# Kernel optimization log

Measured on AMD Instinct MI355X. Metric: run time of the kernel, lower is better.

## Reference

```python
import jax, jax.numpy as jnp
import numpy as np

HEADS = 8
D_MODEL = 512
NU = 1
EPS = 1e-6
SEQ = 4096
BATCH = 8
DK = D_MODEL // HEADS          # 64
PHI = 2 * NU * DK              # 128, DPFP output dim


def dpfp(x):
    """Deterministic Parameter-Free Projection, then L1 normalize."""
    x = jnp.concatenate([jax.nn.relu(x), jax.nn.relu(-x)], axis=-1)  # [..., 2*dk]
    x_rolled = jnp.concatenate([jnp.roll(x, j, axis=-1) for j in range(1, NU + 1)], axis=-1)
    x_repeat = jnp.concatenate([x] * NU, axis=-1)
    y = x_repeat * x_rolled                                          # [..., 2*nu*dk]
    return y / (jnp.sum(y, axis=-1, keepdims=True) + EPS)


def setup_inputs() -> dict:
    key = jax.random.key(0)
    ks = jax.random.split(key, 7)
    s = 0.02
    return {
        "x": jax.random.normal(ks[0], (SEQ, BATCH, D_MODEL), dtype=jnp.float32),
        "Wq": jax.random.normal(ks[1], (D_MODEL, HEADS * DK), dtype=jnp.float32) * s,
        "Wk": jax.random.normal(ks[2], (D_MODEL, HEADS * DK), dtype=jnp.float32) * s,
        "Wv": jax.random.normal(ks[3], (D_MODEL, HEADS * DK), dtype=jnp.float32) * s,
        "Wg": jax.random.normal(ks[4], (D_MODEL, HEADS), dtype=jnp.float32) * s,
        "Wo": jax.random.normal(ks[5], (D_MODEL, D_MODEL), dtype=jnp.float32) * s,
        "bo": jnp.zeros((D_MODEL,), dtype=jnp.float32),
    }


def reference(x, Wq, Wk, Wv, Wg, Wo, bo):
    S, B, D = x.shape
    q = dpfp((x @ Wq).reshape(S, B, HEADS, DK))            # [S,B,H,PHI]
    k = dpfp((x @ Wk).reshape(S, B, HEADS, DK))            # [S,B,H,PHI]
    v = (x @ Wv).reshape(S, B, HEADS, DK)                  # [S,B,H,DK]
    beta = jax.nn.sigmoid((x @ Wg).reshape(S, B, HEADS, 1))  # [S,B,H,1]

    def step(W, qkvb):
        qi, ki, vi, bi = qkvb                              # [B,H,PHI],[B,H,PHI],[B,H,DK],[B,H,1]
        v_exist = jnp.einsum('bhvk,bhk->bhv', W, ki)       # delta-rule read
        W = W + jnp.einsum('bhv,bhk->bhvk', bi * (vi - v_exist), ki)
        out = jnp.einsum('bhvk,bhk->bhv', W, qi)
        return W, out

    W0 = jnp.zeros((B, HEADS, DK, PHI), dtype=x.dtype)
    _, outs = jax.lax.scan(step, W0, (q, k, v, beta))      # outs: [S,B,H,DK]
    out = outs.reshape(S, B, HEADS * DK)
    return out @ Wo + bo
```

## Files before the change

kernel.cpp:

```cpp
#include <hip/hip_runtime.h>

#define SEQ 4096
#define BATCH 8
#define HEADS 8
#define DMODEL 512
#define DK 64
#define PHI 128
#define CHUNK 1024
#define CROWS (CHUNK * BATCH)
#define SB 32
#define NSB (CHUNK / SB)

__device__ __forceinline__ void async16(const float* g, float* l)
{
    __builtin_amdgcn_global_load_lds((const __attribute__((address_space(1))) void*)g,
                                     (__attribute__((address_space(3))) void*)l, 16, 0, 0);
}
__device__ __forceinline__ void async4(const float* g, float* l)
{
    __builtin_amdgcn_global_load_lds((const __attribute__((address_space(1))) void*)g,
                                     (__attribute__((address_space(3))) void*)l, 4, 0, 0);
}

__device__ __forceinline__ float rowsum16(float x)
{
    x += __int_as_float(__builtin_amdgcn_update_dpp(0, __float_as_int(x), 0x121, 0xF, 0xF, true));
    x += __int_as_float(__builtin_amdgcn_update_dpp(0, __float_as_int(x), 0x122, 0xF, 0xF, true));
    x += __int_as_float(__builtin_amdgcn_update_dpp(0, __float_as_int(x), 0x124, 0xF, 0xF, true));
    x += __int_as_float(__builtin_amdgcn_update_dpp(0, __float_as_int(x), 0x128, 0xF, 0xF, true));
    return x;
}

__device__ __forceinline__ float dot8(const float4 x0, const float4 x1,
                                      const float4 y0, const float4 y1)
{
    float a  = x0.x * y0.x;
    float b2 = x1.x * y1.x;
    a = fmaf(x0.y, y0.y, a); b2 = fmaf(x1.y, y1.y, b2);
    a = fmaf(x0.z, y0.z, a); b2 = fmaf(x1.z, y1.z, b2);
    a = fmaf(x0.w, y0.w, a); b2 = fmaf(x1.w, y1.w, b2);
    return a + b2;
}

__global__ __launch_bounds__(256)
void transpose_kernel(const float* __restrict__ X, float* __restrict__ XT)
{
    __shared__ float tile[64][65];
    const int t  = threadIdx.x;
    const int tx = t & 15;
    const int ty = t >> 4;
    const int bm = blockIdx.x * 64;
    const int bn = blockIdx.y * 64;
#pragma unroll
    for (int i = 0; i < 4; ++i) {
        const int r = ty + i * 16;
        const float4 v = *(const float4*)(X + (size_t)(bm + r) * 512 + bn + tx * 4);
        tile[r][tx * 4 + 0] = v.x; tile[r][tx * 4 + 1] = v.y;
        tile[r][tx * 4 + 2] = v.z; tile[r][tx * 4 + 3] = v.w;
    }
    __syncthreads();
#pragma unroll
    for (int i = 0; i < 4; ++i) {
        const int r = ty + i * 16;
        float4 v;
        v.x = tile[tx * 4 + 0][r];
        v.y = tile[tx * 4 + 1][r];
        v.z = tile[tx * 4 + 2][r];
        v.w = tile[tx * 4 + 3][r];
        *(float4*)(XT + (size_t)(bn + r) * CROWS + bm + tx * 4) = v;
    }
}

__global__ __launch_bounds__(256)
void gemm_qkv(const float* __restrict__ AT,
              const float* __restrict__ Wq, const float* __restrict__ Wk,
              const float* __restrict__ Wv,
              float* __restrict__ Qp, float* __restrict__ Kp, float* __restrict__ Vd)
{
    __shared__ __align__(16) float As[2][16][128];
    __shared__ __align__(16) float Bs[2][16][128];
    const int t  = threadIdx.x;
    const int tx = t & 15;
    const int ty = t >> 4;
    const int bm  = blockIdx.x * 128;
    const int grp = blockIdx.y >> 2;
    const int bn  = (blockIdx.y & 3) * 128;
    const float* B = (grp == 0) ? Wq : (grp == 1) ? Wk : Wv;

    float acc[8][8];
#pragma unroll
    for (int i = 0; i < 8; ++i)
#pragma unroll
        for (int j = 0; j < 8; ++j) acc[i][j] = 0.f;

    auto stage = [&](int buf, int kt) {
        const int k0 = kt * 16;
#pragma unroll
        for (int i = 0; i < 2; ++i) {
            const int L = t + i * 256;
            const int k = L >> 5, c4 = L & 31;
            async16(AT + (size_t)(k0 + k) * CROWS + bm + c4 * 4,
                    &As[buf][0][0] + L * 4);
            async16(B + (size_t)(k0 + k) * 512 + bn + c4 * 4,
                    &Bs[buf][0][0] + L * 4);
        }
    };

    stage(0, 0);
    for (int kt = 0; kt < 32; ++kt) {
        const int buf = kt & 1;
        __syncthreads();
        if (kt + 1 < 32) stage(buf ^ 1, kt + 1);
#pragma unroll
        for (int k = 0; k < 16; ++k) {
            float af[8], bf[8];
            *(float4*)&af[0] = *(const float4*)&As[buf][k][ty * 8];
            *(float4*)&af[4] = *(const float4*)&As[buf][k][ty * 8 + 4];
            *(float4*)&bf[0] = *(const float4*)&Bs[buf][k][tx * 4];
            *(float4*)&bf[4] = *(const float4*)&Bs[buf][k][64 + tx * 4];
#pragma unroll
            for (int i = 0; i < 8; ++i)
#pragma unroll
                for (int j = 0; j < 8; ++j)
                    acc[i][j] = fmaf(af[i], bf[j], acc[i][j]);
        }
    }

    if (grp < 2) {
        float* dst = grp ? Kp : Qp;
        const int ln  = t & 63;
        const int lnp = (ln & 48) | ((ln + 15) & 15);
        const int hA  = bn >> 6;
#pragma unroll
        for (int hh = 0; hh < 2; ++hh) {
            const int h = hA + hh;
#pragma unroll
            for (int i = 0; i < 8; ++i) {
                const int m = bm + ty * 8 + i;
                float ap[4], an[4];
#pragma unroll
                for (int j = 0; j < 4; ++j) {
                    const float v = acc[i][hh * 4 + j];
                    ap[j] = fmaxf(v, 0.f);
                    an[j] = fmaxf(-v, 0.f);
                }
                const float sap = __shfl(ap[3], lnp);
                const float san = __shfl(an[3], lnp);
                const float p0  = (tx == 0) ? san : sap;
                const float p64 = (tx == 0) ? sap : san;
                float y0[4], y1[4];
                y0[0] = ap[0] * p0;    y1[0] = an[0] * p64;
                y0[1] = ap[1] * ap[0]; y1[1] = an[1] * an[0];
                y0[2] = ap[2] * ap[1]; y1[2] = an[2] * an[1];
                y0[3] = ap[3] * ap[2]; y1[3] = an[3] * an[2];
                float s = (y0[0] + y0[1] + y0[2] + y0[3]) + (y1[0] + y1[1] + y1[2] + y1[3]);
                s = rowsum16(s);
                const float inv = 1.f / (s + 1e-6f);
                float4 o0, o1;
                o0.x = y0[0] * inv; o0.y = y0[1] * inv; o0.z = y0[2] * inv; o0.w = y0[3] * inv;
                o1.x = y1[0] * inv; o1.y = y1[1] * inv; o1.z = y1[2] * inv; o1.w = y1[3] * inv;
                *(float4*)(dst + (size_t)m * 1024 + h * 128 + tx * 4)      = o0;
                *(float4*)(dst + (size_t)m * 1024 + h * 128 + 64 + tx * 4) = o1;
            }
        }
    } else {
#pragma unroll
        for (int i = 0; i < 8; ++i) {
            const int m = bm + ty * 8 + i;
            float4 o0, o1;
            o0.x = acc[i][0]; o0.y = acc[i][1]; o0.z = acc[i][2]; o0.w = acc[i][3];
            o1.x = acc[i][4]; o1.y = acc[i][5]; o1.z = acc[i][6]; o1.w = acc[i][7];
            *(float4*)(Vd + (size_t)m * 512 + bn + tx * 4)      = o0;
            *(float4*)(Vd + (size_t)m * 512 + bn + 64 + tx * 4) = o1;
        }
    }
}

__global__ __launch_bounds__(256)
void gemm_wo(const float* __restrict__ AT, const float* __restrict__ B,
             const float* __restrict__ bias, float* __restrict__ C)
{
    __shared__ __align__(16) float As[2][32][128];
    __shared__ __align__(16) float Bs[2][32][64];
    const int t  = threadIdx.x;
    const int tx = t & 15;
    const int ty = t >> 4;
    const int bm = blockIdx.x * 128;
    const int bn = blockIdx.y * 64;

    float acc[8][4];
#pragma unroll
    for (int i = 0; i < 8; ++i)
#pragma unroll
        for (int j = 0; j < 4; ++j) acc[i][j] = 0.f;

    auto stage = [&](int buf, int kt) {
        const int k0 = kt * 32;
#pragma unroll
        for (int i = 0; i < 4; ++i) {
            const int L = t + i * 256;
            const int k = L >> 5, c4 = L & 31;
            async16(AT + (size_t)(k0 + k) * CROWS + bm + c4 * 4,
                    &As[buf][0][0] + L * 4);
        }
#pragma unroll
        for (int i = 0; i < 2; ++i) {
            const int L = t + i * 256;
            const int k = L >> 4, c4 = L & 15;
            async16(B + (size_t)(k0 + k) * 512 + bn + c4 * 4,
                    &Bs[buf][0][0] + L * 4);
        }
    };

    stage(0, 0);
    for (int kt = 0; kt < 16; ++kt) {
        const int buf = kt & 1;
        __syncthreads();
        if (kt + 1 < 16) stage(buf ^ 1, kt + 1);
#pragma unroll
        for (int k = 0; k < 32; ++k) {
            float af[8], bf[4];
            *(float4*)&af[0] = *(const float4*)&As[buf][k][ty * 8];
            *(float4*)&af[4] = *(const float4*)&As[buf][k][ty * 8 + 4];
            *(float4*)&bf[0] = *(const float4*)&Bs[buf][k][tx * 4];
#pragma unroll
            for (int i = 0; i < 8; ++i)
#pragma unroll
                for (int j = 0; j < 4; ++j)
                    acc[i][j] = fmaf(af[i], bf[j], acc[i][j]);
        }
    }

#pragma unroll
    for (int i = 0; i < 8; ++i) {
        const int m = bm + ty * 8 + i;
        float4 o;
        o.x = acc[i][0]; o.y = acc[i][1]; o.z = acc[i][2]; o.w = acc[i][3];
        const float4 bb = *(const float4*)(bias + bn + tx * 4);
        o.x += bb.x; o.y += bb.y; o.z += bb.z; o.w += bb.w;
        *(float4*)(C + (size_t)m * 512 + bn + tx * 4) = o;
    }
}

__global__ __launch_bounds__(256)
void gemm_g_kernel(const float* __restrict__ X, const float* __restrict__ Wg,
                   float* __restrict__ Bt)
{
    const int idx = blockIdx.x * 256 + threadIdx.x;
    const int row = idx >> 3;
    const int c   = idx & 7;
    const float4* x4 = (const float4*)(X + (size_t)row * DMODEL);
    float acc = 0.f;
    for (int k4 = 0; k4 < 128; ++k4) {
        const float4 xv = x4[k4];
        acc = fmaf(xv.x, Wg[(k4 * 4 + 0) * 8 + c], acc);
        acc = fmaf(xv.y, Wg[(k4 * 4 + 1) * 8 + c], acc);
        acc = fmaf(xv.z, Wg[(k4 * 4 + 2) * 8 + c], acc);
        acc = fmaf(xv.w, Wg[(k4 * 4 + 3) * 8 + c], acc);
    }
    Bt[idx] = 1.f / (1.f + expf(-acc));
}

__global__ __launch_bounds__(256)
void scan_kernel(const float* __restrict__ Qp, const float* __restrict__ Kp,
                 const float* __restrict__ Vd, const float* __restrict__ Bt,
                 float* __restrict__ outsT, float* __restrict__ Wst,
                 int s0, int first)
{
    const int blk = blockIdx.x;
    const int bh  = blk & 63;
    const int rg  = blk >> 6;
    const int b   = bh >> 3;
    const int h   = bh & 7;
    const int t   = threadIdx.x;
    const int c      = t & 15;
    const int rloc   = t >> 4;
    const int wv  = t >> 6;
    const int ln  = t & 63;

    __shared__ __align__(16) float sk[2][SB][PHI];
    __shared__ __align__(16) float sq[2][SB][PHI];
    __shared__ __align__(16) float sv[2][SB][16];
    __shared__ __align__(16) float sb2[2][SB];
    __shared__ __align__(16) float sd[2][SB][4];

    const size_t bh128 = (size_t)(b * 8 + h) * 128;

    float w[8];
    float* wslot = Wst + (size_t)blk * 2048 + t * 8;
    if (first) {
#pragma unroll
        for (int j = 0; j < 8; ++j) w[j] = 0.f;
    } else {
        const float4 w0 = *(const float4*)(wslot);
        const float4 w1 = *(const float4*)(wslot + 4);
        w[0] = w0.x; w[1] = w0.y; w[2] = w0.z; w[3] = w0.w;
        w[4] = w1.x; w[5] = w1.y; w[6] = w1.z; w[7] = w1.w;
    }

    auto stage = [&](int sbuf, int sb) {
        const int sqb = sb * SB;
        if (wv < 2) {
#pragma unroll
            for (int i = 0; i < 8; ++i) {
                const int L  = i * 128 + wv * 64 + ln;
                const int sl = L >> 5, c4 = L & 31;
                async16(Kp + (size_t)(sqb + sl) * 8192 + bh128 + c4 * 4,
                        &sk[sbuf][0][0] + L * 4);
            }
            {
                const int L  = wv * 64 + ln;
                const int sl = L >> 2, c4 = L & 3;
                async16(Vd + (size_t)(sqb + sl) * 4096 + b * 512 + h * 64 + rg * 16 + c4 * 4,
                        &sv[sbuf][0][0] + L * 4);
            }
        } else {
#pragma unroll
            for (int i = 0; i < 8; ++i) {
                const int L  = i * 128 + (wv - 2) * 64 + ln;
                const int sl = L >> 5, c4 = L & 31;
                async16(Qp + (size_t)(sqb + sl) * 8192 + bh128 + c4 * 4,
                        &sq[sbuf][0][0] + L * 4);
            }
            if (wv == 2 && ln < SB) {
                async4(Bt + (size_t)(s0 + sqb + ln) * 64 + b * 8 + h,
                       &sb2[sbuf][0] + ln);
            }
        }
    };

    auto dots_phase = [&](int buf, int sb) {
        const int sl0 = 2 * rloc;
        const float* kmp = (rloc == 0) ? &sk[buf ^ 1][SB - 1][0] : &sk[buf][sl0 - 1][0];
        const float4 km0 = *(const float4*)(kmp + 4 * c);
        const float4 km1 = *(const float4*)(kmp + 64 + 4 * c);
        const float4 ka0 = *(const float4*)&sk[buf][sl0][4 * c];
        const float4 ka1 = *(const float4*)&sk[buf][sl0][64 + 4 * c];
        const float4 kb0 = *(const float4*)&sk[buf][sl0 + 1][4 * c];
        const float4 kb1 = *(const float4*)&sk[buf][sl0 + 1][64 + 4 * c];
        const float4 qa0 = *(const float4*)&sq[buf][sl0][4 * c];
        const float4 qa1 = *(const float4*)&sq[buf][sl0][64 + 4 * c];
        const float4 qb0 = *(const float4*)&sq[buf][sl0 + 1][4 * c];
        const float4 qb1 = *(const float4*)&sq[buf][sl0 + 1][64 + 4 * c];
        const float kk_a  = rowsum16(dot8(km0, km1, ka0, ka1));
        const float kq1_a = rowsum16(dot8(km0, km1, qa0, qa1));
        const float kq0_a = rowsum16(dot8(ka0, ka1, qa0, qa1));
        const float kk_b  = rowsum16(dot8(ka0, ka1, kb0, kb1));
        const float kq1_b = rowsum16(dot8(ka0, ka1, qb0, qb1));
        const float kq0_b = rowsum16(dot8(kb0, kb1, qb0, qb1));
        if (c == 0) {
            const bool z = (sb == 0) && (rloc == 0);
            sd[buf][sl0][0] = z ? 0.f : kk_a;
            sd[buf][sl0][1] = z ? 0.f : kq1_a;
            sd[buf][sl0][2] = kq0_a;
            sd[buf][sl0][3] = sb2[buf][sl0];
            sd[buf][sl0 + 1][0] = kk_b;
            sd[buf][sl0 + 1][1] = kq1_b;
            sd[buf][sl0 + 1][2] = kq0_b;
            sd[buf][sl0 + 1][3] = sb2[buf][sl0 + 1];
        }
    };

    struct Frag { float4 k0, k1, q0, q1; float bb, bv, kk, kq1, kq0; };
    Frag r[8];
    float d_prev = 0.f;

    auto preload = [&](Frag& f, int sbuf, int sl) {
        f.k0 = *(const float4*)&sk[sbuf][sl][4 * c];
        f.k1 = *(const float4*)&sk[sbuf][sl][64 + 4 * c];
        f.q0 = *(const float4*)&sq[sbuf][sl][4 * c];
        f.q1 = *(const float4*)&sq[sbuf][sl][64 + 4 * c];
        const float4 dd = *(const float4*)&sd[sbuf][sl][0];
        f.kk = dd.x; f.kq1 = dd.y; f.kq0 = dd.z; f.bb = dd.w;
        f.bv = f.bb * sv[sbuf][sl][rloc];
    };

    auto step_compute = [&](const Frag& f, const Frag& fp, int g) {
        float A0 = w[0] * f.k0.x;
        float A1 = w[4] * f.k1.x;
        A0 = fmaf(w[1], f.k0.y, A0); A1 = fmaf(w[5], f.k1.y, A1);
        A0 = fmaf(w[2], f.k0.z, A0); A1 = fmaf(w[6], f.k1.z, A1);
        A0 = fmaf(w[3], f.k0.w, A0); A1 = fmaf(w[7], f.k1.w, A1);
        float Q0 = w[0] * f.q0.x;
        float Q1 = w[4] * f.q1.x;
        Q0 = fmaf(w[1], f.q0.y, Q0); Q1 = fmaf(w[5], f.q1.y, Q1);
        Q0 = fmaf(w[2], f.q0.z, Q0); Q1 = fmaf(w[6], f.q1.z, Q1);
        Q0 = fmaf(w[3], f.q0.w, Q0); Q1 = fmaf(w[7], f.q1.w, Q1);
        const float Ar  = rowsum16(A0 + A1);
        const float Aqr = rowsum16(Q0 + Q1);
        w[0] = fmaf(d_prev, fp.k0.x, w[0]);
        w[1] = fmaf(d_prev, fp.k0.y, w[1]);
        w[2] = fmaf(d_prev, fp.k0.z, w[2]);
        w[3] = fmaf(d_prev, fp.k0.w, w[3]);
        w[4] = fmaf(d_prev, fp.k1.x, w[4]);
        w[5] = fmaf(d_prev, fp.k1.y, w[5]);
        w[6] = fmaf(d_prev, fp.k1.z, w[6]);
        w[7] = fmaf(d_prev, fp.k1.w, w[7]);
        const float a = fmaf(d_prev, f.kk, Ar);
        const float d = fmaf(-f.bb, a, f.bv);
        float o = fmaf(d_prev, f.kq1, Aqr);
        o = fmaf(d, f.kq0, o);
        if (c == 0)
            outsT[(size_t)(h * DK + rg * 16 + rloc) * CROWS + g * BATCH + b] = o;
        d_prev = d;
    };

    r[7].k0 = make_float4(0.f, 0.f, 0.f, 0.f);
    r[7].k1 = make_float4(0.f, 0.f, 0.f, 0.f);

    stage(0, 0);
    for (int sb = 0; sb < NSB; ++sb) {
        const int buf = sb & 1;
        __syncthreads();
        dots_phase(buf, sb);
        __syncthreads();
        if (sb + 1 < NSB) stage(buf ^ 1, sb + 1);
        preload(r[0], buf, 0);
        preload(r[1], buf, 1);
        preload(r[2], buf, 2);
        preload(r[3], buf, 3);
#pragma unroll
        for (int s = 0; s < SB; ++s) {
            if (s + 4 < SB) preload(r[(s + 4) & 7], buf, s + 4);
            step_compute(r[s & 7], r[(s + 7) & 7], sb * SB + s);
        }
    }

    w[0] = fmaf(d_prev, r[7].k0.x, w[0]);
    w[1] = fmaf(d_prev, r[7].k0.y, w[1]);
    w[2] = fmaf(d_prev, r[7].k0.z, w[2]);
    w[3] = fmaf(d_prev, r[7].k0.w, w[3]);
    w[4] = fmaf(d_prev, r[7].k1.x, w[4]);
    w[5] = fmaf(d_prev, r[7].k1.y, w[5]);
    w[6] = fmaf(d_prev, r[7].k1.z, w[6]);
    w[7] = fmaf(d_prev, r[7].k1.w, w[7]);

    float4 w0, w1;
    w0.x = w[0]; w0.y = w[1]; w0.z = w[2]; w0.w = w[3];
    w1.x = w[4]; w1.y = w[5]; w1.z = w[6]; w1.w = w[7];
    *(float4*)(wslot)     = w0;
    *(float4*)(wslot + 4) = w1;
}

extern "C" void kernel_launch(void* const* d_in, const int* in_sizes, int n_in,
                              void* d_out, int out_size, void* d_ws, size_t ws_size,
                              hipStream_t stream)
{
    const float* x  = (const float*)d_in[0];
    const float* Wq = (const float*)d_in[1];
    const float* Wk = (const float*)d_in[2];
    const float* Wv = (const float*)d_in[3];
    const float* Wg = (const float*)d_in[4];
    const float* Wo = (const float*)d_in[5];
    const float* bo = (const float*)d_in[6];
    float* out = (float*)d_out;

    float* ws  = (float*)d_ws;
    float* XTc = ws;
    float* tmp = ws;
    float* Qp  = ws  + (size_t)512 * CROWS;
    float* Kp  = Qp  + (size_t)CROWS * 1024;
    float* Vd  = Kp  + (size_t)CROWS * 1024;
    float* Bt  = Vd  + (size_t)CROWS * 512;
    float* Wst = Bt  + (size_t)(SEQ * BATCH) * 8;
    (void)in_sizes; (void)n_in; (void)out_size; (void)ws_size;

    const dim3 gt(CROWS / 64, DMODEL / 64);
    const dim3 gq(CROWS / 128, 12);
    const dim3 go(CROWS / 128, DMODEL / 64);
    const int NCH = SEQ / CHUNK;

    gemm_g_kernel<<<(SEQ * BATCH * 8) / 256, 256, 0, stream>>>(x, Wg, Bt);

    for (int c = 0; c < NCH; ++c) {
        const float* xc = x + (size_t)c * CROWS * DMODEL;
        transpose_kernel<<<gt, 256, 0, stream>>>(xc, XTc);
        gemm_qkv<<<gq, 256, 0, stream>>>(XTc, Wq, Wk, Wv, Qp, Kp, Vd);
        scan_kernel<<<256, 256, 0, stream>>>(Qp, Kp, Vd, Bt, tmp, Wst,
                                             c * CHUNK, c == 0 ? 1 : 0);
        gemm_wo<<<go, 256, 0, stream>>>(tmp, Wo, bo,
                                        out + (size_t)c * CROWS * DMODEL);
    }
}
```

Measured before the change: 1.615 ms.

## Use split-bf16 MFMA for QKV projection and drop the transpose kernel

Replaces the FP32 FMA QKV GEMM with MFMA bf16 16x16x32 instructions. Each FP32 operand is split into high and low bf16 parts and three products are summed to keep near-FP32 accuracy. The GEMM now reads x row-major directly and converts it in registers before writing to LDS, so the separate transpose kernel and its workspace round trip are removed. The cost is splitting overhead, three MFMAs per tile, register-staged global loads instead of async LDS loads, and scalar output stores instead of float4 stores.

```diff
diff --git a/kernel.cpp b/kernel.cpp
--- a/kernel.cpp
+++ b/kernel.cpp
@@ -11,6 +11,9 @@
 #define SB 32
 #define NSB (CHUNK / SB)
 
+typedef float f32x4 __attribute__((ext_vector_type(4)));
+typedef short s16x8 __attribute__((ext_vector_type(8)));
+
 __device__ __forceinline__ void async16(const float* g, float* l)
 {
     __builtin_amdgcn_global_load_lds((const __attribute__((address_space(1))) void*)g,
@@ -42,136 +45,182 @@
     return a + b2;
 }
 
+__device__ __forceinline__ unsigned packhi2(unsigned a, unsigned b)
+{
+    return (b & 0xFFFF0000u) | (a >> 16);
+}
+
 __global__ __launch_bounds__(256)
-void transpose_kernel(const float* __restrict__ X, float* __restrict__ XT)
-{
-    __shared__ float tile[64][65];
-    const int t  = threadIdx.x;
-    const int tx = t & 15;
-    const int ty = t >> 4;
-    const int bm = blockIdx.x * 64;
-    const int bn = blockIdx.y * 64;
-#pragma unroll
-    for (int i = 0; i < 4; ++i) {
-        const int r = ty + i * 16;
-        const float4 v = *(const float4*)(X + (size_t)(bm + r) * 512 + bn + tx * 4);
-        tile[r][tx * 4 + 0] = v.x; tile[r][tx * 4 + 1] = v.y;
-        tile[r][tx * 4 + 2] = v.z; tile[r][tx * 4 + 3] = v.w;
-    }
-    __syncthreads();
-#pragma unroll
-    for (int i = 0; i < 4; ++i) {
-        const int r = ty + i * 16;
-        float4 v;
-        v.x = tile[tx * 4 + 0][r];
-        v.y = tile[tx * 4 + 1][r];
-        v.z = tile[tx * 4 + 2][r];
-        v.w = tile[tx * 4 + 3][r];
-        *(float4*)(XT + (size_t)(bn + r) * CROWS + bm + tx * 4) = v;
-    }
-}
-
-__global__ __launch_bounds__(256)
-void gemm_qkv(const float* __restrict__ AT,
-              const float* __restrict__ Wq, const float* __restrict__ Wk,
-              const float* __restrict__ Wv,
-              float* __restrict__ Qp, float* __restrict__ Kp, float* __restrict__ Vd)
-{
-    __shared__ __align__(16) float As[2][16][128];
-    __shared__ __align__(16) float Bs[2][16][128];
-    const int t  = threadIdx.x;
-    const int tx = t & 15;
-    const int ty = t >> 4;
-    const int bm  = blockIdx.x * 128;
-    const int grp = blockIdx.y >> 2;
-    const int bn  = (blockIdx.y & 3) * 128;
-    const float* B = (grp == 0) ? Wq : (grp == 1) ? Wk : Wv;
-
-    float acc[8][8];
-#pragma unroll
-    for (int i = 0; i < 8; ++i)
-#pragma unroll
-        for (int j = 0; j < 8; ++j) acc[i][j] = 0.f;
-
-    auto stage = [&](int buf, int kt) {
-        const int k0 = kt * 16;
-#pragma unroll
-        for (int i = 0; i < 2; ++i) {
+void gemm_qkv_mfma(const float* __restrict__ x,
+                   const float* __restrict__ Wq, const float* __restrict__ Wk,
+                   const float* __restrict__ Wv,
+                   float* __restrict__ Qp, float* __restrict__ Kp, float* __restrict__ Vd)
+{
+    __shared__ __align__(16) unsigned short Ah[2][128][40];
+    __shared__ __align__(16) unsigned short Al[2][128][40];
+    __shared__ __align__(16) float          Bs[2][32][132];
+
+    const int t    = threadIdx.x;
+    const int l    = t & 63;
+    const int wv   = t >> 6;
+    const int wm   = wv >> 1;
+    const int wn   = wv & 1;
+    const int tx16 = l & 15;
+    const int g4   = l >> 4;
+    const int bm   = blockIdx.x * 128;
+    const int grp  = blockIdx.y >> 2;
+    const int bn   = (blockIdx.y & 3) * 128;
+    const float* W = (grp == 0) ? Wq : (grp == 1) ? Wk : Wv;
+
+    f32x4 acc[4][4];
+#pragma unroll
+    for (int i = 0; i < 4; ++i)
+#pragma unroll
+        for (int j = 0; j < 4; ++j) acc[i][j] = 0.f;
+
+    float4 xr[4], wr[4];
+
+    auto loadA = [&](int kt) {
+#pragma unroll
+        for (int i = 0; i < 4; ++i) {
             const int L = t + i * 256;
-            const int k = L >> 5, c4 = L & 31;
-            async16(AT + (size_t)(k0 + k) * CROWS + bm + c4 * 4,
-                    &As[buf][0][0] + L * 4);
-            async16(B + (size_t)(k0 + k) * 512 + bn + c4 * 4,
-                    &Bs[buf][0][0] + L * 4);
-        }
-    };
-
-    stage(0, 0);
-    for (int kt = 0; kt < 32; ++kt) {
+            const int row = L >> 3, kq = (L & 7) << 2;
+            xr[i] = *(const float4*)(x + (size_t)(bm + row) * 512 + kt * 32 + kq);
+        }
+    };
+    auto writeA = [&](int buf) {
+#pragma unroll
+        for (int i = 0; i < 4; ++i) {
+            const int L = t + i * 256;
+            const int row = L >> 3, kq = (L & 7) << 2;
+            const float4 v = xr[i];
+            const unsigned u0 = __float_as_uint(v.x), u1 = __float_as_uint(v.y);
+            const unsigned u2 = __float_as_uint(v.z), u3 = __float_as_uint(v.w);
+            const float l0 = v.x - __uint_as_float(u0 & 0xFFFF0000u);
+            const float l1 = v.y - __uint_as_float(u1 & 0xFFFF0000u);
+            const float l2 = v.z - __uint_as_float(u2 & 0xFFFF0000u);
+            const float l3 = v.w - __uint_as_float(u3 & 0xFFFF0000u);
+            *(uint2*)&Ah[buf][row][kq] =
+                make_uint2(packhi2(u0, u1), packhi2(u2, u3));
+            *(uint2*)&Al[buf][row][kq] =
+                make_uint2(packhi2(__float_as_uint(l0), __float_as_uint(l1)),
+                           packhi2(__float_as_uint(l2), __float_as_uint(l3)));
+        }
+    };
+    auto loadB = [&](int kt) {
+#pragma unroll
+        for (int i = 0; i < 4; ++i) {
+            const int L = t + i * 256;
+            const int k = L >> 5, c4 = (L & 31) << 2;
+            wr[i] = *(const float4*)(W + (size_t)(kt * 32 + k) * 512 + bn + c4);
+        }
+    };
+    auto writeB = [&](int buf) {
+#pragma unroll
+        for (int i = 0; i < 4; ++i) {
+            const int L = t + i * 256;
+            const int k = L >> 5, c4 = (L & 31) << 2;
+            *(float4*)&Bs[buf][k][c4] = wr[i];
+        }
+    };
+
+    auto compute = [&](int buf) {
+        s16x8 ah[4], al[4];
+#pragma unroll
+        for (int mf = 0; mf < 4; ++mf) {
+            const int rowA = wm * 64 + mf * 16 + tx16;
+            ah[mf] = *(const s16x8*)&Ah[buf][rowA][g4 * 8];
+            al[mf] = *(const s16x8*)&Al[buf][rowA][g4 * 8];
+        }
+#pragma unroll
+        for (int nf = 0; nf < 4; ++nf) {
+            const int ncol = wn * 64 + nf * 16 + tx16;
+            float bv[8];
+#pragma unroll
+            for (int i = 0; i < 8; ++i) bv[i] = Bs[buf][g4 * 8 + i][ncol];
+            unsigned uh[4], ul[4];
+#pragma unroll
+            for (int w2 = 0; w2 < 4; ++w2) {
+                const unsigned ua = __float_as_uint(bv[2 * w2]);
+                const unsigned ub = __float_as_uint(bv[2 * w2 + 1]);
+                const float la = bv[2 * w2]     - __uint_as_float(ua & 0xFFFF0000u);
+                const float lb = bv[2 * w2 + 1] - __uint_as_float(ub & 0xFFFF0000u);
+                uh[w2] = packhi2(ua, ub);
+                ul[w2] = packhi2(__float_as_uint(la), __float_as_uint(lb));
+            }
+            int4 bhv = make_int4(uh[0], uh[1], uh[2], uh[3]);
+            int4 blv = make_int4(ul[0], ul[1], ul[2], ul[3]);
+            const s16x8 bh = *(const s16x8*)&bhv;
+            const s16x8 bl = *(const s16x8*)&blv;
+#pragma unroll
+            for (int mf = 0; mf < 4; ++mf) {
+                acc[mf][nf] = __builtin_amdgcn_mfma_f32_16x16x32_bf16(ah[mf], bh, acc[mf][nf], 0, 0, 0);
+                acc[mf][nf] = __builtin_amdgcn_mfma_f32_16x16x32_bf16(ah[mf], bl, acc[mf][nf], 0, 0, 0);
+                acc[mf][nf] = __builtin_amdgcn_mfma_f32_16x16x32_bf16(al[mf], bh, acc[mf][nf], 0, 0, 0);
+            }
+        }
+    };
+
+    loadA(0); loadB(0); writeA(0); writeB(0);
+    for (int kt = 0; kt < 16; ++kt) {
         const int buf = kt & 1;
         __syncthreads();
-        if (kt + 1 < 32) stage(buf ^ 1, kt + 1);
-#pragma unroll
-        for (int k = 0; k < 16; ++k) {
-            float af[8], bf[8];
-            *(float4*)&af[0] = *(const float4*)&As[buf][k][ty * 8];
-            *(float4*)&af[4] = *(const float4*)&As[buf][k][ty * 8 + 4];
-            *(float4*)&bf[0] = *(const float4*)&Bs[buf][k][tx * 4];
-            *(float4*)&bf[4] = *(const float4*)&Bs[buf][k][64 + tx * 4];
-#pragma unroll
-            for (int i = 0; i < 8; ++i)
-#pragma unroll
-                for (int j = 0; j < 8; ++j)
-                    acc[i][j] = fmaf(af[i], bf[j], acc[i][j]);
-        }
+        if (kt < 15) { loadA(kt + 1); loadB(kt + 1); }
+        compute(buf);
+        if (kt < 15) { writeA(buf ^ 1); writeB(buf ^ 1); }
     }
 
     if (grp < 2) {
         float* dst = grp ? Kp : Qp;
-        const int ln  = t & 63;
-        const int lnp = (ln & 48) | ((ln + 15) & 15);
-        const int hA  = bn >> 6;
-#pragma unroll
-        for (int hh = 0; hh < 2; ++hh) {
-            const int h = hA + hh;
-#pragma unroll
-            for (int i = 0; i < 8; ++i) {
-                const int m = bm + ty * 8 + i;
-                float ap[4], an[4];
-#pragma unroll
-                for (int j = 0; j < 4; ++j) {
-                    const float v = acc[i][hh * 4 + j];
-                    ap[j] = fmaxf(v, 0.f);
-                    an[j] = fmaxf(-v, 0.f);
+        const int h = (blockIdx.y & 3) * 2 + wn;
+        const int prevl = (l & 48) | ((l + 15) & 15);
+#pragma unroll
+        for (int mf = 0; mf < 4; ++mf) {
+#pragma unroll
+            for (int j = 0; j < 4; ++j) {
+                float ap[4], an[4], sap[4], san[4];
+#pragma unroll
+                for (int nf = 0; nf < 4; ++nf) {
+                    const float v = acc[mf][nf][j];
+                    ap[nf] = fmaxf(v, 0.f);
+                    an[nf] = fmaxf(-v, 0.f);
                 }
-                const float sap = __shfl(ap[3], lnp);
-                const float san = __shfl(an[3], lnp);
-                const float p0  = (tx == 0) ? san : sap;
-                const float p64 = (tx == 0) ? sap : san;
+#pragma unroll
+                for (int nf = 0; nf < 4; ++nf) {
+                    sap[nf] = __shfl(ap[nf], prevl);
+                    san[nf] = __shfl(an[nf], prevl);
+                }
                 float y0[4], y1[4];
-                y0[0] = ap[0] * p0;    y1[0] = an[0] * p64;
-                y0[1] = ap[1] * ap[0]; y1[1] = an[1] * an[0];
-                y0[2] = ap[2] * ap[1]; y1[2] = an[2] * an[1];
-                y0[3] = ap[3] * ap[2]; y1[3] = an[3] * an[2];
+#pragma unroll
+                for (int nf = 0; nf < 4; ++nf) {
+                    const float pa = (tx16 == 0) ? (nf ? sap[nf - 1] : san[3]) : sap[nf];
+                    const float pn = (tx16 == 0) ? (nf ? san[nf - 1] : sap[3]) : san[nf];
+                    y0[nf] = ap[nf] * pa;
+                    y1[nf] = an[nf] * pn;
+                }
                 float s = (y0[0] + y0[1] + y0[2] + y0[3]) + (y1[0] + y1[1] + y1[2] + y1[3]);
                 s = rowsum16(s);
                 const float inv = 1.f / (s + 1e-6f);
-                float4 o0, o1;
-                o0.x = y0[0] * inv; o0.y = y0[1] * inv; o0.z = y0[2] * inv; o0.w = y0[3] * inv;
-                o1.x = y1[0] * inv; o1.y = y1[1] * inv; o1.z = y1[2] * inv; o1.w = y1[3] * inv;
-                *(float4*)(dst + (size_t)m * 1024 + h * 128 + tx * 4)      = o0;
-                *(float4*)(dst + (size_t)m * 1024 + h * 128 + 64 + tx * 4) = o1;
+                const int m = bm + wm * 64 + mf * 16 + g4 * 4 + j;
+#pragma unroll
+                for (int nf = 0; nf < 4; ++nf) {
+                    dst[(size_t)m * 1024 + h * 128 + nf * 16 + tx16]      = y0[nf] * inv;
+                    dst[(size_t)m * 1024 + h * 128 + 64 + nf * 16 + tx16] = y1[nf] * inv;
+                }
             }
         }
     } else {
 #pragma unroll
-        for (int i = 0; i < 8; ++i) {
-            const int m = bm + ty * 8 + i;
-            float4 o0, o1;
-            o0.x = acc[i][0]; o0.y = acc[i][1]; o0.z = acc[i][2]; o0.w = acc[i][3];
-            o1.x = acc[i][4]; o1.y = acc[i][5]; o1.z = acc[i][6]; o1.w = acc[i][7];
-            *(float4*)(Vd + (size_t)m * 512 + bn + tx * 4)      = o0;
-            *(float4*)(Vd + (size_t)m * 512 + bn + 64 + tx * 4) = o1;
+        for (int mf = 0; mf < 4; ++mf) {
+#pragma unroll
+            for (int j = 0; j < 4; ++j) {
+                const int m = bm + wm * 64 + mf * 16 + g4 * 4 + j;
+#pragma unroll
+                for (int nf = 0; nf < 4; ++nf) {
+                    Vd[(size_t)m * 512 + (blockIdx.y & 3) * 128 + wn * 64 + nf * 16 + tx16] =
+                        acc[mf][nf][j];
+                }
+            }
         }
     }
 }
@@ -456,7 +505,6 @@
     float* out = (float*)d_out;
 
     float* ws  = (float*)d_ws;
-    float* XTc = ws;
     float* tmp = ws;
     float* Qp  = ws  + (size_t)512 * CROWS;
     float* Kp  = Qp  + (size_t)CROWS * 1024;
@@ -465,7 +513,6 @@
     float* Wst = Bt  + (size_t)(SEQ * BATCH) * 8;
     (void)in_sizes; (void)n_in; (void)out_size; (void)ws_size;
 
-    const dim3 gt(CROWS / 64, DMODEL / 64);
     const dim3 gq(CROWS / 128, 12);
     const dim3 go(CROWS / 128, DMODEL / 64);
     const int NCH = SEQ / CHUNK;
@@ -474,8 +521,7 @@
 
     for (int c = 0; c < NCH; ++c) {
         const float* xc = x + (size_t)c * CROWS * DMODEL;
-        transpose_kernel<<<gt, 256, 0, stream>>>(xc, XTc);
-        gemm_qkv<<<gq, 256, 0, stream>>>(XTc, Wq, Wk, Wv, Qp, Kp, Vd);
+        gemm_qkv_mfma<<<gq, 256, 0, stream>>>(xc, Wq, Wk, Wv, Qp, Kp, Vd);
         scan_kernel<<<256, 256, 0, stream>>>(Qp, Kp, Vd, Bt, tmp, Wst,
                                              c * CHUNK, c == 0 ? 1 : 0);
         gemm_wo<<<go, 256, 0, stream>>>(tmp, Wo, bo,
```

New measurement: 1.324 ms. -18.0%, faster.
